# Kernel tuning notes

Hardware: AMD Instinct MI355X
Metric: run time of the kernel (lower is better)

## Reference

```python
import jax, jax.numpy as jnp
import numpy as np

D_MODEL = 1024
N_HEAD = 16
B, S = 4, 1024


def setup_inputs() -> dict:
    key = jax.random.key(0)
    ks = jax.random.split(key, 10)
    f = lambda k, shp: jax.random.normal(k, shp, dtype=jnp.float32)
    return {
        "x": f(ks[0], (B, S, D_MODEL)),
        "y": f(ks[1], (B, S, D_MODEL)),
        "z": f(ks[2], (B, S, D_MODEL)),
        "mask": f(ks[3], (1, 1, S, S)) * 0.1,
        "wq_w": f(ks[4], (D_MODEL, D_MODEL)) * (D_MODEL ** -0.5),
        "wq_b": f(ks[5], (D_MODEL,)) * 0.02,
        "wk_w": f(ks[6], (D_MODEL, D_MODEL)) * (D_MODEL ** -0.5),
        "wk_b": f(ks[7], (D_MODEL,)) * 0.02,
        "wv_w": f(ks[8], (D_MODEL, D_MODEL)) * (D_MODEL ** -0.5),
        "wv_b": f(ks[9], (D_MODEL,)) * 0.02,
    }


def reference(x, y, z, mask, wq_w, wq_b, wk_w, wk_b, wv_w, wv_b):
    b, xl, d = x.shape
    hd = d // N_HEAD
    # linear projections (torch Linear: x @ W^T + b)
    q = x @ wq_w.T + wq_b
    k = y @ wk_w.T + wk_b
    v = z @ wv_w.T + wv_b
    # [B, H, L, hd]
    q = q.reshape(b, xl, N_HEAD, hd).transpose(0, 2, 1, 3)
    k = k.reshape(b, y.shape[1], N_HEAD, hd).transpose(0, 2, 1, 3)
    v = v.reshape(b, z.shape[1], N_HEAD, hd).transpose(0, 2, 1, 3)
    # NOTE: source scales by sqrt(d_model), not sqrt(head_dim)
    scale = 1.0 / jnp.sqrt(jnp.asarray(d, dtype=x.dtype))
    logits = jnp.einsum("bhqd,bhkd->bhqk", q, k) * scale
    score = jax.nn.softmax(logits, axis=-1)
    # mask added AFTER softmax (faithful to source)
    score = score + mask
    out = jnp.einsum("bhqk,bhkd->bhqd", score, v)
    return out.transpose(0, 2, 1, 3).reshape(b, xl, d)
```

## Files before the change

### kernel.cpp

```cpp
#include <hip/hip_runtime.h>
#include <hip/hip_bf16.h>
#include <cstdint>

typedef __bf16 bf16_t;
typedef __bf16 bf16x8 __attribute__((ext_vector_type(8)));
typedef __bf16 bf16x4 __attribute__((ext_vector_type(4)));
typedef float floatx4 __attribute__((ext_vector_type(4)));

typedef __attribute__((address_space(3))) uint32_t lds_u32_t;
typedef const __attribute__((address_space(1))) uint32_t g_u32_t;

#define MFMA_BF16(a, b, c) __builtin_amdgcn_mfma_f32_16x16x32_bf16((a), (b), (c), 0, 0, 0)

static constexpr int S = 1024;
static constexpr int HD = 64;

struct ConvArgs {
  const float* src[7];
  bf16_t* dst[7];
  int n[7];
};

__global__ __launch_bounds__(256) void convert_kernel(ConvArgs a) {
  const int j = blockIdx.y;
  const float4* __restrict__ s = (const float4*)a.src[j];
  bf16x4* __restrict__ d = (bf16x4*)a.dst[j];
  const int n4 = a.n[j] >> 2;
  for (int i = blockIdx.x * blockDim.x + threadIdx.x; i < n4; i += gridDim.x * blockDim.x) {
    float4 v = s[i];
    bf16x4 o;
    o[0] = (bf16_t)v.x; o[1] = (bf16_t)v.y; o[2] = (bf16_t)v.z; o[3] = (bf16_t)v.w;
    d[i] = o;
  }
}

struct GemmCfg {
  const bf16_t* A;
  const bf16_t* Bm;
  void* out;
  const float* bias;
  int mode;
};

union GemmSmem {
  struct { bf16_t A[128 * 64]; bf16_t B[128 * 64]; } ab;
  bf16_t C[128 * 136];
};

__global__ __launch_bounds__(256, 3) void gemm_nt_kernel(GemmCfg c0, GemmCfg c1, GemmCfg c2, int K) {
  GemmCfg cfg = (blockIdx.y == 0) ? c0 : (blockIdx.y == 1 ? c1 : c2);
  __shared__ GemmSmem u;
  __shared__ float bias_s[128];
  const int tid = threadIdx.x;
  const int wave = tid >> 6;
  const int lane = tid & 63;
  const int g = lane >> 4;
  const int cl = lane & 15;
  const int mq = (wave & 1) * 64;
  const int nq = (wave >> 1) * 64;

  const int xcd = blockIdx.x & 7, idx = blockIdx.x >> 3;
  int mb, nb;
  if (cfg.mode == 0) { mb = xcd * 4 + (idx & 3); nb = idx >> 2; }
  else               { nb = xcd * 4 + (idx & 3); mb = idx >> 2; }
  const int m0 = mb * 128, n0 = nb * 128;

  if (tid < 128) bias_s[tid] = cfg.bias[(cfg.mode == 0 ? n0 : m0) + tid];

  const int srow = tid >> 3;
  const int sch = (tid & 7) ^ (srow & 7);
  const bf16_t* Ag = cfg.A + (size_t)(m0 + srow) * K + sch * 8;
  const bf16_t* Bg = cfg.Bm + (size_t)(n0 + srow) * K + sch * 8;
  const int swz = cl & 7;

  floatx4 acc[4][4];
#pragma unroll
  for (int i = 0; i < 4; ++i)
#pragma unroll
    for (int j = 0; j < 4; ++j) acc[i][j] = floatx4{0.f, 0.f, 0.f, 0.f};

  const int kiters = K >> 6;
  for (int kt = 0; kt < kiters; ++kt) {
    __syncthreads();
#pragma unroll
    for (int i = 0; i < 4; ++i) {
      __builtin_amdgcn_global_load_lds((g_u32_t*)(const void*)(Ag + (size_t)(i * 32) * K),
                                       (lds_u32_t*)(void*)&u.ab.A[(i * 256 + tid) * 8], 16, 0, 0);
      __builtin_amdgcn_global_load_lds((g_u32_t*)(const void*)(Bg + (size_t)(i * 32) * K),
                                       (lds_u32_t*)(void*)&u.ab.B[(i * 256 + tid) * 8], 16, 0, 0);
    }
    Ag += 64;
    Bg += 64;
    __syncthreads();

#pragma unroll
    for (int kc = 0; kc < 2; ++kc) {
      bf16x8 af[4], bfr[4];
#pragma unroll
      for (int i = 0; i < 4; ++i)
        af[i] = *(const bf16x8*)&u.ab.A[(mq + i * 16 + cl) * 64 + ((kc * 4 + g) ^ swz) * 8];
#pragma unroll
      for (int j = 0; j < 4; ++j)
        bfr[j] = *(const bf16x8*)&u.ab.B[(nq + j * 16 + cl) * 64 + ((kc * 4 + g) ^ swz) * 8];
#pragma unroll
      for (int i = 0; i < 4; ++i)
#pragma unroll
        for (int j = 0; j < 4; ++j) acc[i][j] = MFMA_BF16(af[i], bfr[j], acc[i][j]);
    }
  }

  __syncthreads();
#pragma unroll
  for (int i = 0; i < 4; ++i)
#pragma unroll
    for (int j = 0; j < 4; ++j)
#pragma unroll
      for (int r = 0; r < 4; ++r) {
        const int ml = mq + i * 16 + g * 4 + r;
        const int nl = nq + j * 16 + cl;
        float v = acc[i][j][r] + bias_s[cfg.mode == 0 ? nl : ml];
        u.C[ml * 136 + nl] = (bf16_t)v;
      }
  __syncthreads();
#pragma unroll
  for (int it = 0; it < 8; ++it) {
    const int ix = it * 256 + tid;
    const int ml = ix >> 4, nc = ix & 15;
    bf16x8 val = *(const bf16x8*)&u.C[ml * 136 + nc * 8];
    const int m = m0 + ml, n = n0 + nc * 8;
    size_t addr;
    if (cfg.mode == 0)
      addr = (size_t)((m >> 10) * 16 + (n >> 6)) * 65536 + (m & 1023) * 64 + (n & 63);
    else
      addr = (size_t)((n >> 10) * 16 + (m >> 6)) * 65536 + (m & 63) * 1024 + (n & 1023);
    *(bf16x8*)&((bf16_t*)cfg.out)[addr] = val;
  }
}

__global__ __launch_bounds__(256, 4) void attn_kernel(const bf16_t* __restrict__ Q,
                                                      const bf16_t* __restrict__ Kb,
                                                      const bf16_t* __restrict__ Vt,
                                                      const bf16_t* __restrict__ Mk,
                                                      float* __restrict__ out) {
  __shared__ bf16_t Ks[64 * 64];
  __shared__ bf16_t Vs[64 * 64];
  __shared__ bf16_t Pbuf[4][16 * 72];
  const int tid = threadIdx.x;
  const int wave = tid >> 6, lane = tid & 63;
  const int g = lane >> 4, cl = lane & 15;
  const int bh = blockIdx.x & 63, qt = blockIdx.x >> 6;
  const int q0w = qt * 64 + wave * 16;
  const bf16_t* Qp = Q + (size_t)bh * (S * HD);
  const bf16_t* Kp = Kb + (size_t)bh * (S * HD);
  const bf16_t* Vp = Vt + (size_t)bh * (S * HD);
  bf16_t* Pw = &Pbuf[wave][0];

  const int srow = tid >> 3, sch = (tid & 7) ^ ((tid >> 3) & 7);
  const int sw = cl & 7;

  bf16x8 qf[2];
#pragma unroll
  for (int kc = 0; kc < 2; ++kc)
    qf[kc] = *(const bf16x8*)&Qp[(size_t)(q0w + cl) * HD + kc * 32 + g * 8];

  floatx4 o[4], o2[4];
#pragma unroll
  for (int nj = 0; nj < 4; ++nj) {
    o[nj] = floatx4{0.f, 0.f, 0.f, 0.f};
    o2[nj] = floatx4{0.f, 0.f, 0.f, 0.f};
  }
  float dsq = 0.f;

  for (int kt = 0; kt < 16; ++kt) {
    const int k0 = kt * 64;

    bf16x8 ma[2];
#pragma unroll
    for (int kc = 0; kc < 2; ++kc)
      ma[kc] = *(const bf16x8*)&Mk[(size_t)(q0w + cl) * S + k0 + kc * 32 + g * 8];

    __syncthreads();
#pragma unroll
    for (int i = 0; i < 2; ++i)
      __builtin_amdgcn_global_load_lds(
          (g_u32_t*)(const void*)&Kp[(size_t)(k0 + i * 32 + srow) * HD + sch * 8],
          (lds_u32_t*)(void*)&Ks[(i * 256 + tid) * 8], 16, 0, 0);
#pragma unroll
    for (int i = 0; i < 2; ++i)
      __builtin_amdgcn_global_load_lds(
          (g_u32_t*)(const void*)&Vp[(size_t)(i * 32 + srow) * S + k0 + sch * 8],
          (lds_u32_t*)(void*)&Vs[(i * 256 + tid) * 8], 16, 0, 0);
    __syncthreads();

#pragma unroll
    for (int mi = 0; mi < 4; ++mi) {
      bf16x8 kf0 = *(const bf16x8*)&Ks[(mi * 16 + cl) * 64 + ((0 + g) ^ sw) * 8];
      bf16x8 kf1 = *(const bf16x8*)&Ks[(mi * 16 + cl) * 64 + ((4 + g) ^ sw) * 8];
      floatx4 s0 = floatx4{0.f, 0.f, 0.f, 0.f};
      s0 = MFMA_BF16(kf0, qf[0], s0);
      s0 = MFMA_BF16(kf1, qf[1], s0);
      bf16x4 p0;
#pragma unroll
      for (int r = 0; r < 4; ++r) {
        float e0 = __expf(s0[r] * 0.03125f);
        dsq += e0;
        p0[r] = (bf16_t)e0;
      }
      *(bf16x4*)&Pw[cl * 72 + mi * 16 + g * 4] = p0;
    }

#pragma unroll
    for (int kc = 0; kc < 2; ++kc) {
      bf16x8 pa = *(const bf16x8*)&Pw[cl * 72 + kc * 32 + g * 8];
#pragma unroll
      for (int nj = 0; nj < 4; ++nj) {
        bf16x8 vf = *(const bf16x8*)&Vs[(nj * 16 + cl) * 64 + ((kc * 4 + g) ^ sw) * 8];
        o[nj] = MFMA_BF16(pa, vf, o[nj]);
        o2[nj] = MFMA_BF16(ma[kc], vf, o2[nj]);
      }
    }
  }

  dsq += __shfl_xor(dsq, 16, 64);
  dsq += __shfl_xor(dsq, 32, 64);

  const int b = bh >> 4, h = bh & 15;
#pragma unroll
  for (int r = 0; r < 4; ++r) {
    float dv = __shfl(dsq, g * 4 + r, 64);
    float dinv = 1.0f / dv;
    const int orow = q0w + g * 4 + r;
#pragma unroll
    for (int nj = 0; nj < 4; ++nj) {
      const int hd = nj * 16 + cl;
      out[((size_t)b * S + orow) * 1024 + h * HD + hd] = o[nj][r] * dinv + o2[nj][r];
    }
  }
}

extern "C" void kernel_launch(void* const* d_in, const int* in_sizes, int n_in,
                              void* d_out, int out_size, void* d_ws, size_t ws_size,
                              hipStream_t stream) {
  const float* x = (const float*)d_in[0];
  const float* y = (const float*)d_in[1];
  const float* z = (const float*)d_in[2];
  const float* mask = (const float*)d_in[3];
  const float* wq_w = (const float*)d_in[4];
  const float* wq_b = (const float*)d_in[5];
  const float* wk_w = (const float*)d_in[6];
  const float* wk_b = (const float*)d_in[7];
  const float* wv_w = (const float*)d_in[8];
  const float* wv_b = (const float*)d_in[9];

  uint8_t* ws = (uint8_t*)d_ws;
  const size_t MB = 1u << 20;
  bf16_t* Xb = (bf16_t*)(ws + 0 * MB);
  bf16_t* Yb = (bf16_t*)(ws + 8 * MB);
  bf16_t* Zb = (bf16_t*)(ws + 16 * MB);
  bf16_t* Wqb = (bf16_t*)(ws + 24 * MB);
  bf16_t* Wkb = (bf16_t*)(ws + 26 * MB);
  bf16_t* Wvb = (bf16_t*)(ws + 28 * MB);
  bf16_t* Mb = (bf16_t*)(ws + 30 * MB);
  bf16_t* Qb = (bf16_t*)(ws + 32 * MB);
  bf16_t* Kb = (bf16_t*)(ws + 40 * MB);
  bf16_t* Vtb = (bf16_t*)(ws + 48 * MB);

  ConvArgs ca;
  ca.src[0] = x;    ca.dst[0] = Xb;  ca.n[0] = 4 * 1024 * 1024;
  ca.src[1] = y;    ca.dst[1] = Yb;  ca.n[1] = 4 * 1024 * 1024;
  ca.src[2] = z;    ca.dst[2] = Zb;  ca.n[2] = 4 * 1024 * 1024;
  ca.src[3] = wq_w; ca.dst[3] = Wqb; ca.n[3] = 1024 * 1024;
  ca.src[4] = wk_w; ca.dst[4] = Wkb; ca.n[4] = 1024 * 1024;
  ca.src[5] = wv_w; ca.dst[5] = Wvb; ca.n[5] = 1024 * 1024;
  ca.src[6] = mask; ca.dst[6] = Mb;  ca.n[6] = 1024 * 1024;
  convert_kernel<<<dim3(512, 7), 256, 0, stream>>>(ca);

  GemmCfg cq{Xb, Wqb, (void*)Qb, wq_b, 0};
  GemmCfg ck{Yb, Wkb, (void*)Kb, wk_b, 0};
  GemmCfg cv{Wvb, Zb, (void*)Vtb, wv_b, 1};
  gemm_nt_kernel<<<dim3(256, 3), 256, 0, stream>>>(cq, ck, cv, 1024);

  attn_kernel<<<dim3(1024), 256, 0, stream>>>(Qb, Kb, Vtb, Mb, (float*)d_out);
}
```

Baseline: 186.3 us.

## Double-buffer K/V tiles in LDS to prefetch the next tile during compute

The attention kernel now keeps two LDS buffers for the K and V tiles. It issues the async global-to-LDS loads for tile kt+1 before computing on tile kt, so there is one barrier per iteration instead of two. This is meant to hide global load latency behind MFMA and softmax work. In exchange, LDS use per block roughly doubles for K/V, and the occupancy hint drops from 4 to 3 blocks per CU, which reduces latency hiding across blocks.

```diff
diff --git a/kernel.cpp b/kernel.cpp
--- a/kernel.cpp
+++ b/kernel.cpp
@@ -137,13 +137,13 @@
   }
 }
 
-__global__ __launch_bounds__(256, 4) void attn_kernel(const bf16_t* __restrict__ Q,
+__global__ __launch_bounds__(256, 3) void attn_kernel(const bf16_t* __restrict__ Q,
                                                       const bf16_t* __restrict__ Kb,
                                                       const bf16_t* __restrict__ Vt,
                                                       const bf16_t* __restrict__ Mk,
                                                       float* __restrict__ out) {
-  __shared__ bf16_t Ks[64 * 64];
-  __shared__ bf16_t Vs[64 * 64];
+  __shared__ bf16_t Ks[2][64 * 64];
+  __shared__ bf16_t Vs[2][64 * 64];
   __shared__ bf16_t Pbuf[4][16 * 72];
   const int tid = threadIdx.x;
   const int wave = tid >> 6, lane = tid & 63;
@@ -158,6 +158,19 @@
   const int srow = tid >> 3, sch = (tid & 7) ^ ((tid >> 3) & 7);
   const int sw = cl & 7;
 
+#define STAGE(BUF, KT)                                                                        \
+  do {                                                                                        \
+    const int k0s = (KT) * 64;                                                                \
+    _Pragma("unroll") for (int i = 0; i < 2; ++i)                                             \
+        __builtin_amdgcn_global_load_lds(                                                     \
+            (g_u32_t*)(const void*)&Kp[(size_t)(k0s + i * 32 + srow) * HD + sch * 8],         \
+            (lds_u32_t*)(void*)&Ks[BUF][(i * 256 + tid) * 8], 16, 0, 0);                      \
+    _Pragma("unroll") for (int i = 0; i < 2; ++i)                                             \
+        __builtin_amdgcn_global_load_lds(                                                     \
+            (g_u32_t*)(const void*)&Vp[(size_t)(i * 32 + srow) * S + k0s + sch * 8],          \
+            (lds_u32_t*)(void*)&Vs[BUF][(i * 256 + tid) * 8], 16, 0, 0);                      \
+  } while (0)
+
   bf16x8 qf[2];
 #pragma unroll
   for (int kc = 0; kc < 2; ++kc)
@@ -171,31 +184,27 @@
   }
   float dsq = 0.f;
 
+  STAGE(0, 0);
+  __syncthreads();
+
+  int cur = 0;
   for (int kt = 0; kt < 16; ++kt) {
     const int k0 = kt * 64;
 
+    if (kt < 15) STAGE(cur ^ 1, kt + 1);
+
     bf16x8 ma[2];
 #pragma unroll
     for (int kc = 0; kc < 2; ++kc)
       ma[kc] = *(const bf16x8*)&Mk[(size_t)(q0w + cl) * S + k0 + kc * 32 + g * 8];
 
-    __syncthreads();
-#pragma unroll
-    for (int i = 0; i < 2; ++i)
-      __builtin_amdgcn_global_load_lds(
-          (g_u32_t*)(const void*)&Kp[(size_t)(k0 + i * 32 + srow) * HD + sch * 8],
-          (lds_u32_t*)(void*)&Ks[(i * 256 + tid) * 8], 16, 0, 0);
-#pragma unroll
-    for (int i = 0; i < 2; ++i)
-      __builtin_amdgcn_global_load_lds(
-          (g_u32_t*)(const void*)&Vp[(size_t)(i * 32 + srow) * S + k0 + sch * 8],
-          (lds_u32_t*)(void*)&Vs[(i * 256 + tid) * 8], 16, 0, 0);
-    __syncthreads();
+    const bf16_t* Kc = &Ks[cur][0];
+    const bf16_t* Vc = &Vs[cur][0];
 
 #pragma unroll
     for (int mi = 0; mi < 4; ++mi) {
-      bf16x8 kf0 = *(const bf16x8*)&Ks[(mi * 16 + cl) * 64 + ((0 + g) ^ sw) * 8];
-      bf16x8 kf1 = *(const bf16x8*)&Ks[(mi * 16 + cl) * 64 + ((4 + g) ^ sw) * 8];
+      bf16x8 kf0 = *(const bf16x8*)&Kc[(mi * 16 + cl) * 64 + ((0 + g) ^ sw) * 8];
+      bf16x8 kf1 = *(const bf16x8*)&Kc[(mi * 16 + cl) * 64 + ((4 + g) ^ sw) * 8];
       floatx4 s0 = floatx4{0.f, 0.f, 0.f, 0.f};
       s0 = MFMA_BF16(kf0, qf[0], s0);
       s0 = MFMA_BF16(kf1, qf[1], s0);
@@ -214,12 +223,16 @@
       bf16x8 pa = *(const bf16x8*)&Pw[cl * 72 + kc * 32 + g * 8];
 #pragma unroll
       for (int nj = 0; nj < 4; ++nj) {
-        bf16x8 vf = *(const bf16x8*)&Vs[(nj * 16 + cl) * 64 + ((kc * 4 + g) ^ sw) * 8];
+        bf16x8 vf = *(const bf16x8*)&Vc[(nj * 16 + cl) * 64 + ((kc * 4 + g) ^ sw) * 8];
         o[nj] = MFMA_BF16(pa, vf, o[nj]);
         o2[nj] = MFMA_BF16(ma[kc], vf, o2[nj]);
       }
     }
-  }
+
+    __syncthreads();
+    cur ^= 1;
+  }
+#undef STAGE
 
   dsq += __shfl_xor(dsq, 16, 64);
   dsq += __shfl_xor(dsq, 32, 64);
```

After: 192.9 us. +3.6%, slower.
